# Kernel optimization log

Hardware: AMD Instinct MI355X
Metric: run time of the kernel (lower is better)

Reference implementation:

```python
import jax, jax.numpy as jnp
import numpy as np

B, IN, H, NOPT = 16384, 4096, 128, 64
GAIN = 0.5  # default control_gains value in the module


def gru_cell(x, h, Wih, Whh, bih, bhh):
    # torch GRU single step; gate order r, z, n
    gi = x @ Wih + bih          # [B, 3H]
    gh = h @ Whh + bhh          # [B, 3H]
    ir, iz, inn = jnp.split(gi, 3, axis=-1)
    hr, hz, hn = jnp.split(gh, 3, axis=-1)
    r = jax.nn.sigmoid(ir + hr)
    z = jax.nn.sigmoid(iz + hz)
    n = jnp.tanh(inn + r * hn)
    return (1.0 - z) * n + z * h


def setup_inputs() -> dict:
    key = jax.random.key(0)
    ks = jax.random.split(key, 12)
    s = lambda k, shape: (jax.random.normal(k, shape, jnp.float32) * 0.05)
    return {
        "obs": jax.random.normal(ks[0], (B, IN), jnp.float32),
        "chosen_option": jax.random.randint(ks[1], (B,), 0, NOPT),
        "h0": jnp.zeros((B, H), jnp.float32),
        "h1": jnp.zeros((B, H), jnp.float32),
        "Wa": s(ks[2], (IN, H)), "ba": jnp.zeros((H,), jnp.float32),
        "Wih0": s(ks[3], (H, 3 * H)), "Whh0": s(ks[4], (H, 3 * H)),
        "bih0": jnp.zeros((3 * H,), jnp.float32), "bhh0": jnp.zeros((3 * H,), jnp.float32),
        "Wih1": s(ks[5], (2 * H, 3 * H)), "Whh1": s(ks[6], (H, 3 * H)),
        "bih1": jnp.zeros((3 * H,), jnp.float32), "bhh1": jnp.zeros((3 * H,), jnp.float32),
        "Wv0": s(ks[7], (H, NOPT)), "bv0": jnp.zeros((NOPT,), jnp.float32),
        "Wv1": s(ks[8], (H, NOPT)), "bv1": jnp.zeros((NOPT,), jnp.float32),
        "Wt0": s(ks[9], (H, NOPT)), "bt0": jnp.zeros((NOPT,), jnp.float32),
    }


def reference(obs, chosen_option, h0, h1, Wa, ba, Wih0, Whh0, bih0, bhh0,
              Wih1, Whh1, bih1, bhh1, Wv0, bv0, Wv1, bv1, Wt0, bt0):
    # attention: tanh(Linear(obs))
    attn = jnp.tanh(obs @ Wa + ba)                       # [B, H]
    # layer 0: GRU on attn
    h0n = gru_cell(attn, h0, Wih0, Whh0, bih0, bhh0)     # [B, H]
    hc0 = (h0n - 0.5) * GAIN + 0.5                       # gain contrast
    v0 = hc0 @ Wv0 + bv0                                 # [B, NOPT]
    term = jax.nn.sigmoid(hc0 @ Wt0 + bt0)               # [B, NOPT]
    term_p = jnp.take_along_axis(term, chosen_option[:, None], axis=1)  # [B, 1]
    # layer 1: GRU on cat(attn, own hidden)
    x1 = jnp.concatenate([attn, h1], axis=-1)            # [B, 2H]
    h1n = gru_cell(x1, h1, Wih1, Whh1, bih1, bhh1)       # [B, H]
    hc1 = (h1n - 0.5) * GAIN + 0.5
    v1 = hc1 @ Wv1 + bv1                                 # [B, NOPT]
    return v0, term_p, v1, h0n, h1n
```

## Files before the change

kernel.cpp:

```cpp
#include <hip/hip_runtime.h>
#include <hip/hip_bf16.h>
#include <stdint.h>


typedef __attribute__((ext_vector_type(8))) short bf16x8;
typedef __attribute__((ext_vector_type(4))) float f32x4;
typedef __attribute__((ext_vector_type(8))) float f32x8;

#define INDIM 4096
#define H 128
#define NOPT 64

#define WS_WAT    0u
#define WS_WIH0T  524288u
#define WS_WHH0T  573440u
#define WS_WIH1T  622592u
#define WS_WHH1T  720896u
#define WS_WV0T   770048u
#define WS_WV1T   778240u
#define WS_WT0T   786432u

#define OUT_V0    0u
#define OUT_TERMP 1048576u
#define OUT_V1    1064960u
#define OUT_H0N   2113536u
#define OUT_H1N   4210688u

static __device__ __forceinline__ uint16_t f2bf(float f) {
  __hip_bfloat16 h = __float2bfloat16(f);
  return __builtin_bit_cast(uint16_t, h);
}
static __device__ __forceinline__ float sigm(float x) { return 1.0f / (1.0f + __expf(-x)); }
static __device__ __forceinline__ float fast_tanh(float x) {
  float e = __expf(2.0f * x);
  return 1.0f - 2.0f / (e + 1.0f);
}
static __device__ __forceinline__ f32x4 mfma16(bf16x8 a, bf16x8 b, f32x4 c) {
  return __builtin_amdgcn_mfma_f32_16x16x32_bf16(a, b, c, 0, 0, 0);
}
static __device__ __forceinline__ bf16x8 cvt8(f32x8 v) {
  bf16x8 r;
#pragma unroll
  for (int j = 0; j < 8; ++j) r[j] = (short)f2bf(v[j]);
  return r;
}

__global__ void k_transpose(const float* __restrict__ Wa,
                            const float* __restrict__ Wih0,
                            const float* __restrict__ Whh0,
                            const float* __restrict__ Wih1,
                            const float* __restrict__ Whh1,
                            const float* __restrict__ Wv0,
                            const float* __restrict__ Wv1,
                            const float* __restrict__ Wt0,
                            uint16_t* __restrict__ ws) {
  __shared__ float sT[32][34];
  int blk = blockIdx.x;
  const float* in; uint16_t* out; int K; int N; int base;
  if (blk < 512)      { in = Wa;   out = ws + WS_WAT;   K = 4096; N = 128; base = 0; }
  else if (blk < 560) { in = Wih0; out = ws + WS_WIH0T; K = 128;  N = 384; base = 512; }
  else if (blk < 608) { in = Whh0; out = ws + WS_WHH0T; K = 128;  N = 384; base = 560; }
  else if (blk < 704) { in = Wih1; out = ws + WS_WIH1T; K = 256;  N = 384; base = 608; }
  else if (blk < 752) { in = Whh1; out = ws + WS_WHH1T; K = 128;  N = 384; base = 704; }
  else if (blk < 760) { in = Wv0;  out = ws + WS_WV0T;  K = 128;  N = 64;  base = 752; }
  else if (blk < 768) { in = Wv1;  out = ws + WS_WV1T;  K = 128;  N = 64;  base = 760; }
  else                { in = Wt0;  out = ws + WS_WT0T;  K = 128;  N = 64;  base = 768; }
  const int tix = blk - base;
  const int nTK = K >> 5;
  const int kt = tix & (nTK - 1);
  const int nt = tix / nTK;
  const int k0 = kt * 32, n0 = nt * 32;
  const int t = threadIdx.x;
#pragma unroll
  for (int i = 0; i < 4; ++i) {
    int e = i * 256 + t, kk = e >> 5, nn = e & 31;
    sT[kk][nn] = in[(size_t)(k0 + kk) * N + n0 + nn];
  }
  __syncthreads();
#pragma unroll
  for (int i = 0; i < 4; ++i) {
    int e = i * 256 + t, nn = e >> 5, kk = e & 31;
    out[(size_t)(n0 + nn) * K + k0 + kk] = f2bf(sT[kk][nn]);
  }
}

__launch_bounds__(256, 4)
__global__ void k_fused(const float* __restrict__ obs,
                        const uint16_t* __restrict__ ws,
                        const float* __restrict__ ba,
                        const float* __restrict__ h0,
                        const float* __restrict__ bih0,
                        const float* __restrict__ bhh0,
                        const float* __restrict__ bv0,
                        const float* __restrict__ bt0,
                        const int* __restrict__ chosen,
                        const float* __restrict__ h1,
                        const float* __restrict__ bih1,
                        const float* __restrict__ bhh1,
                        const float* __restrict__ bv1,
                        float* __restrict__ out) {
  __shared__ uint16_t sObs[2][16 * 16 * 8];
  __shared__ uint16_t sX[16 * 16 * 8];
  __shared__ uint16_t sC[16 * 16 * 8];
  const uint16_t* WaT   = ws + WS_WAT;
  const uint16_t* Wih0T = ws + WS_WIH0T;
  const uint16_t* Whh0T = ws + WS_WHH0T;
  const uint16_t* Wih1T = ws + WS_WIH1T;
  const uint16_t* Whh1T = ws + WS_WHH1T;
  const uint16_t* Wv0T  = ws + WS_WV0T;
  const uint16_t* Wv1T  = ws + WS_WV1T;
  const uint16_t* Wt0T  = ws + WS_WT0T;
  const int t = threadIdx.x, w = t >> 6, lane = t & 63;
  const int l15 = lane & 15, quad = lane >> 4;
  const int row0 = blockIdx.x * 16;
  const int nbA = 2 * w;

  f32x4 acc0 = {}, acc1 = {};
  {
    const int r16 = t >> 4;
    const int kb16 = t & 15;
    const float* aptr = obs + (size_t)(row0 + r16) * INDIM + kb16 * 8;
    const int wslot = (r16 * 16 + (kb16 ^ r16)) * 8;
    const uint16_t* brow0 = WaT + (size_t)(nbA * 16 + l15) * INDIM + quad * 8;
    const uint16_t* brow1 = brow0 + (size_t)16 * INDIM;
    f32x8 stg = *(const f32x8*)(aptr);
    for (int kt = 0; kt < 32; ++kt) {
      *(bf16x8*)&sObs[kt & 1][wslot] = cvt8(stg);
      if (kt < 31) stg = *(const f32x8*)(aptr + (size_t)(kt + 1) * 128);
      bf16x8 b[8];
      const int kO = kt * 128;
#pragma unroll
      for (int s = 0; s < 4; ++s) {
        b[s]     = *(const bf16x8*)(brow0 + kO + s * 32);
        b[4 + s] = *(const bf16x8*)(brow1 + kO + s * 32);
      }
      __syncthreads();
#pragma unroll
      for (int s = 0; s < 4; ++s) {
        bf16x8 afr = *(const bf16x8*)&sObs[kt & 1][(l15 * 16 + ((s * 4 + quad) ^ l15)) * 8];
        acc0 = mfma16(afr, b[s], acc0);
        acc1 = mfma16(afr, b[4 + s], acc1);
      }
    }
  }
#pragma unroll
  for (int nbl = 0; nbl < 2; ++nbl) {
    const f32x4 A = nbl ? acc1 : acc0;
    const int col = (nbA + nbl) * 16 + l15;
    const float bav = ba[col];
    const int kb = col >> 3;
#pragma unroll
    for (int i = 0; i < 4; ++i) {
      const int r = quad * 4 + i;
      sX[(r * 16 + (kb ^ r)) * 8 + (col & 7)] = f2bf(fast_tanh(A[i] + bav));
    }
  }
  __syncthreads();

  bf16x8 ax[4], ah[4];
  {
    const float* hrow = h0 + (size_t)(row0 + l15) * H + quad * 8;
#pragma unroll
    for (int ks = 0; ks < 4; ++ks) {
      const int kb = ks * 4 + quad;
      ax[ks] = *(const bf16x8*)&sX[(l15 * 16 + (kb ^ l15)) * 8];
      ah[ks] = cvt8(*(const f32x8*)(hrow + ks * 32));
    }
  }
#pragma unroll
  for (int nbl = 0; nbl < 2; ++nbl) {
    const int nrow = (nbA + nbl) * 16 + l15;
    f32x4 air = {}, ahr = {}, aiz = {}, ahz = {}, ain = {}, ahn = {};
#pragma unroll
    for (int ks = 0; ks < 4; ++ks) {
      const int k = ks * 32 + quad * 8;
      bf16x8 b;
      b = *(const bf16x8*)(Wih0T + (size_t)(nrow      ) * H + k); air = mfma16(ax[ks], b, air);
      b = *(const bf16x8*)(Wih0T + (size_t)(nrow + 128) * H + k); aiz = mfma16(ax[ks], b, aiz);
      b = *(const bf16x8*)(Wih0T + (size_t)(nrow + 256) * H + k); ain = mfma16(ax[ks], b, ain);
      b = *(const bf16x8*)(Whh0T + (size_t)(nrow      ) * H + k); ahr = mfma16(ah[ks], b, ahr);
      b = *(const bf16x8*)(Whh0T + (size_t)(nrow + 128) * H + k); ahz = mfma16(ah[ks], b, ahz);
      b = *(const bf16x8*)(Whh0T + (size_t)(nrow + 256) * H + k); ahn = mfma16(ah[ks], b, ahn);
    }
    const int col = nrow;
    const float b_ir = bih0[col],       b_hr = bhh0[col];
    const float b_iz = bih0[col + 128], b_hz = bhh0[col + 128];
    const float b_in = bih0[col + 256], b_hn = bhh0[col + 256];
    const int kb = col >> 3;
#pragma unroll
    for (int i = 0; i < 4; ++i) {
      const int r = quad * 4 + i;
      const int grow = row0 + r;
      const float rr = sigm(air[i] + ahr[i] + b_ir + b_hr);
      const float zz = sigm(aiz[i] + ahz[i] + b_iz + b_hz);
      const float nn = fast_tanh(ain[i] + b_in + rr * (ahn[i] + b_hn));
      const float hv = h0[(size_t)grow * H + col];
      const float hnew = (1.0f - zz) * nn + zz * hv;
      out[OUT_H0N + (size_t)grow * H + col] = hnew;
      sC[(r * 16 + (kb ^ r)) * 8 + (col & 7)] = f2bf(0.5f * hnew + 0.25f);
    }
  }
  __syncthreads();

  {
    int ch[4];
#pragma unroll
    for (int i = 0; i < 4; ++i) ch[i] = chosen[row0 + quad * 4 + i];
    bf16x8 ac[4];
#pragma unroll
    for (int ks = 0; ks < 4; ++ks) {
      const int kb = ks * 4 + quad;
      ac[ks] = *(const bf16x8*)&sC[(l15 * 16 + (kb ^ l15)) * 8];
    }
    f32x4 av = {}, at = {};
    const int nrow = w * 16 + l15;
#pragma unroll
    for (int ks = 0; ks < 4; ++ks) {
      const int k = ks * 32 + quad * 8;
      bf16x8 b;
      b = *(const bf16x8*)(Wv0T + (size_t)nrow * H + k); av = mfma16(ac[ks], b, av);
      b = *(const bf16x8*)(Wt0T + (size_t)nrow * H + k); at = mfma16(ac[ks], b, at);
    }
    const int col = nrow;
    const float bvv = bv0[col], btv = bt0[col];
#pragma unroll
    for (int i = 0; i < 4; ++i) {
      const int grow = row0 + quad * 4 + i;
      out[OUT_V0 + (size_t)grow * NOPT + col] = av[i] + bvv;
      if (ch[i] == col)
        out[OUT_TERMP + grow] = sigm(at[i] + btv);
    }
  }
  __syncthreads();

  bf16x8 ah1[4];
  {
    const float* hrow = h1 + (size_t)(row0 + l15) * H + quad * 8;
#pragma unroll
    for (int ks = 0; ks < 4; ++ks)
      ah1[ks] = cvt8(*(const f32x8*)(hrow + ks * 32));
  }
#pragma unroll
  for (int nbl = 0; nbl < 2; ++nbl) {
    const int nrow = (nbA + nbl) * 16 + l15;
    f32x4 air = {}, ahr = {}, aiz = {}, ahz = {}, ain = {}, ahn = {};
#pragma unroll
    for (int ks = 0; ks < 8; ++ks) {
      const int k = ks * 32 + quad * 8;
      const bf16x8 a = (ks < 4) ? ax[ks] : ah1[ks - 4];
      bf16x8 b;
      b = *(const bf16x8*)(Wih1T + (size_t)(nrow      ) * 256 + k); air = mfma16(a, b, air);
      b = *(const bf16x8*)(Wih1T + (size_t)(nrow + 128) * 256 + k); aiz = mfma16(a, b, aiz);
      b = *(const bf16x8*)(Wih1T + (size_t)(nrow + 256) * 256 + k); ain = mfma16(a, b, ain);
    }
#pragma unroll
    for (int ks = 0; ks < 4; ++ks) {
      const int k = ks * 32 + quad * 8;
      bf16x8 b;
      b = *(const bf16x8*)(Whh1T + (size_t)(nrow      ) * H + k); ahr = mfma16(ah1[ks], b, ahr);
      b = *(const bf16x8*)(Whh1T + (size_t)(nrow + 128) * H + k); ahz = mfma16(ah1[ks], b, ahz);
      b = *(const bf16x8*)(Whh1T + (size_t)(nrow + 256) * H + k); ahn = mfma16(ah1[ks], b, ahn);
    }
    const int col = nrow;
    const float b_ir = bih1[col],       b_hr = bhh1[col];
    const float b_iz = bih1[col + 128], b_hz = bhh1[col + 128];
    const float b_in = bih1[col + 256], b_hn = bhh1[col + 256];
    const int kb = col >> 3;
#pragma unroll
    for (int i = 0; i < 4; ++i) {
      const int r = quad * 4 + i;
      const int grow = row0 + r;
      const float rr = sigm(air[i] + ahr[i] + b_ir + b_hr);
      const float zz = sigm(aiz[i] + ahz[i] + b_iz + b_hz);
      const float nn = fast_tanh(ain[i] + b_in + rr * (ahn[i] + b_hn));
      const float hv = h1[(size_t)grow * H + col];
      const float hnew = (1.0f - zz) * nn + zz * hv;
      out[OUT_H1N + (size_t)grow * H + col] = hnew;
      sC[(r * 16 + (kb ^ r)) * 8 + (col & 7)] = f2bf(0.5f * hnew + 0.25f);
    }
  }
  __syncthreads();

  {
    bf16x8 ac[4];
#pragma unroll
    for (int ks = 0; ks < 4; ++ks) {
      const int kb = ks * 4 + quad;
      ac[ks] = *(const bf16x8*)&sC[(l15 * 16 + (kb ^ l15)) * 8];
    }
    f32x4 av = {};
    const int nrow = w * 16 + l15;
#pragma unroll
    for (int ks = 0; ks < 4; ++ks) {
      const int k = ks * 32 + quad * 8;
      bf16x8 b = *(const bf16x8*)(Wv1T + (size_t)nrow * H + k);
      av = mfma16(ac[ks], b, av);
    }
    const int col = nrow;
    const float bvv = bv1[col];
#pragma unroll
    for (int i = 0; i < 4; ++i) {
      const int grow = row0 + quad * 4 + i;
      out[OUT_V1 + (size_t)grow * NOPT + col] = av[i] + bvv;
    }
  }
}

extern "C" void kernel_launch(void* const* d_in, const int* in_sizes, int n_in,
                              void* d_out, int out_size, void* d_ws, size_t ws_size,
                              hipStream_t stream) {
  (void)in_sizes; (void)n_in; (void)out_size; (void)ws_size;
  const float* obs    = (const float*)d_in[0];
  const int*   chosen = (const int*)d_in[1];
  const float* h0     = (const float*)d_in[2];
  const float* h1     = (const float*)d_in[3];
  const float* Wa     = (const float*)d_in[4];
  const float* ba     = (const float*)d_in[5];
  const float* Wih0   = (const float*)d_in[6];
  const float* Whh0   = (const float*)d_in[7];
  const float* bih0   = (const float*)d_in[8];
  const float* bhh0   = (const float*)d_in[9];
  const float* Wih1   = (const float*)d_in[10];
  const float* Whh1   = (const float*)d_in[11];
  const float* bih1   = (const float*)d_in[12];
  const float* bhh1   = (const float*)d_in[13];
  const float* Wv0    = (const float*)d_in[14];
  const float* bv0    = (const float*)d_in[15];
  const float* Wv1    = (const float*)d_in[16];
  const float* bv1    = (const float*)d_in[17];
  const float* Wt0    = (const float*)d_in[18];
  const float* bt0    = (const float*)d_in[19];
  uint16_t* ws  = (uint16_t*)d_ws;
  float*    out = (float*)d_out;

  hipLaunchKernelGGL(k_transpose, dim3(776), dim3(256), 0, stream,
                     Wa, Wih0, Whh0, Wih1, Whh1, Wv0, Wv1, Wt0, ws);
  hipLaunchKernelGGL(k_fused, dim3(1024), dim3(256), 0, stream,
                     obs, ws, ba, h0, bih0, bhh0, bv0, bt0, chosen,
                     h1, bih1, bhh1, bv1, out);
}
```

Before: 521.1 us.

## Split fused kernel into attention GEMM and GRU kernels with LDS-staged weights

```diff
diff --git a/kernel.cpp b/kernel.cpp
--- a/kernel.cpp
+++ b/kernel.cpp
@@ -19,12 +19,19 @@
 #define WS_WV0T   770048u
 #define WS_WV1T   778240u
 #define WS_WT0T   786432u
+#define WS_ATTN   794624u
 
 #define OUT_V0    0u
 #define OUT_TERMP 1048576u
 #define OUT_V1    1064960u
 #define OUT_H0N   2113536u
 #define OUT_H1N   4210688u
+
+typedef __attribute__((address_space(1))) const void gas_t;
+typedef __attribute__((address_space(3))) void las_t;
+static __device__ __forceinline__ void gll16(const void* g, void* l) {
+  __builtin_amdgcn_global_load_lds((gas_t*)g, (las_t*)l, 16, 0, 0);
+}
 
 static __device__ __forceinline__ uint16_t f2bf(float f) {
   __hip_bfloat16 h = __float2bfloat16(f);
@@ -85,24 +92,89 @@
 }
 
 __launch_bounds__(256, 4)
-__global__ void k_fused(const float* __restrict__ obs,
-                        const uint16_t* __restrict__ ws,
-                        const float* __restrict__ ba,
-                        const float* __restrict__ h0,
-                        const float* __restrict__ bih0,
-                        const float* __restrict__ bhh0,
-                        const float* __restrict__ bv0,
-                        const float* __restrict__ bt0,
-                        const int* __restrict__ chosen,
-                        const float* __restrict__ h1,
-                        const float* __restrict__ bih1,
-                        const float* __restrict__ bhh1,
-                        const float* __restrict__ bv1,
-                        float* __restrict__ out) {
-  __shared__ uint16_t sObs[2][16 * 16 * 8];
-  __shared__ uint16_t sX[16 * 16 * 8];
-  __shared__ uint16_t sC[16 * 16 * 8];
-  const uint16_t* WaT   = ws + WS_WAT;
+__global__ void k_attn(const float* __restrict__ obs,
+                       uint16_t* __restrict__ ws,
+                       const float* __restrict__ ba) {
+  __shared__ __align__(16) uint16_t sA[2][32 * 8 * 8];
+  __shared__ __align__(16) uint16_t sB[2][128 * 8 * 8];
+  const uint16_t* WaT = ws + WS_WAT;
+  uint16_t* attn = ws + WS_ATTN;
+  const int t = threadIdx.x, w = t >> 6, lane = t & 63;
+  const int l15 = lane & 15, quad = lane >> 4;
+  const int wm = w >> 1, wn = w & 1;
+  const int row0 = blockIdx.x * 32;
+  const int rA = wm * 16 + l15;
+  const int sr = t >> 3, sg = t & 7;
+  const float* aSrc = obs + (size_t)(row0 + sr) * INDIM + sg * 8;
+  const int aDst = (sr * 8 + (sg ^ (sr & 7))) * 8;
+  const int n0 = w * 32 + (lane >> 3);
+  const int gsrc = (lane & 7) ^ (n0 & 7);
+  const uint16_t* bSrc = WaT + (size_t)n0 * INDIM + gsrc * 8;
+
+  f32x4 acc[4] = {};
+
+  auto compute = [&](int buf) {
+#pragma unroll
+    for (int ks = 0; ks < 2; ++ks) {
+      bf16x8 a = *(const bf16x8*)&sA[buf][(rA * 8 + ((ks * 4 + quad) ^ (rA & 7))) * 8];
+#pragma unroll
+      for (int nb = 0; nb < 4; ++nb) {
+        const int n = wn * 64 + nb * 16 + l15;
+        bf16x8 b = *(const bf16x8*)&sB[buf][(n * 8 + ((ks * 4 + quad) ^ (n & 7))) * 8];
+        acc[nb] = mfma16(a, b, acc[nb]);
+      }
+    }
+  };
+
+  {
+    f32x8 av = *(const f32x8*)aSrc;
+#pragma unroll
+    for (int j = 0; j < 4; ++j)
+      gll16(bSrc + (size_t)j * 8 * INDIM, (void*)&sB[0][(w * 4 + j) * 512]);
+    *(bf16x8*)&sA[0][aDst] = cvt8(av);
+  }
+  __syncthreads();
+
+  for (int kt = 0; kt < 63; ++kt) {
+    const int cur = kt & 1, nxt = cur ^ 1;
+    f32x8 av = *(const f32x8*)(aSrc + (size_t)(kt + 1) * 64);
+#pragma unroll
+    for (int j = 0; j < 4; ++j)
+      gll16(bSrc + (size_t)(kt + 1) * 64 + (size_t)j * 8 * INDIM,
+            (void*)&sB[nxt][(w * 4 + j) * 512]);
+    compute(cur);
+    *(bf16x8*)&sA[nxt][aDst] = cvt8(av);
+    __syncthreads();
+  }
+  compute(1);
+
+#pragma unroll
+  for (int nb = 0; nb < 4; ++nb) {
+    const int col = wn * 64 + nb * 16 + l15;
+    const float bav = ba[col];
+#pragma unroll
+    for (int i = 0; i < 4; ++i) {
+      const int r = wm * 16 + quad * 4 + i;
+      attn[(size_t)(row0 + r) * H + col] = f2bf(fast_tanh(acc[nb][i] + bav));
+    }
+  }
+}
+
+__launch_bounds__(512, 4)
+__global__ void k_gru(const uint16_t* __restrict__ ws,
+                      const float* __restrict__ h0,
+                      const float* __restrict__ bih0,
+                      const float* __restrict__ bhh0,
+                      const float* __restrict__ bv0,
+                      const float* __restrict__ bt0,
+                      const int* __restrict__ chosen,
+                      const float* __restrict__ h1,
+                      const float* __restrict__ bih1,
+                      const float* __restrict__ bhh1,
+                      const float* __restrict__ bv1,
+                      float* __restrict__ out) {
+  __shared__ __align__(16) uint16_t sC[64 * 16 * 8];
+  const uint16_t* attn  = ws + WS_ATTN;
   const uint16_t* Wih0T = ws + WS_WIH0T;
   const uint16_t* Whh0T = ws + WS_WHH0T;
   const uint16_t* Wih1T = ws + WS_WIH1T;
@@ -112,64 +184,21 @@
   const uint16_t* Wt0T  = ws + WS_WT0T;
   const int t = threadIdx.x, w = t >> 6, lane = t & 63;
   const int l15 = lane & 15, quad = lane >> 4;
-  const int row0 = blockIdx.x * 16;
-  const int nbA = 2 * w;
-
-  f32x4 acc0 = {}, acc1 = {};
-  {
-    const int r16 = t >> 4;
-    const int kb16 = t & 15;
-    const float* aptr = obs + (size_t)(row0 + r16) * INDIM + kb16 * 8;
-    const int wslot = (r16 * 16 + (kb16 ^ r16)) * 8;
-    const uint16_t* brow0 = WaT + (size_t)(nbA * 16 + l15) * INDIM + quad * 8;
-    const uint16_t* brow1 = brow0 + (size_t)16 * INDIM;
-    f32x8 stg = *(const f32x8*)(aptr);
-    for (int kt = 0; kt < 32; ++kt) {
-      *(bf16x8*)&sObs[kt & 1][wslot] = cvt8(stg);
-      if (kt < 31) stg = *(const f32x8*)(aptr + (size_t)(kt + 1) * 128);
-      bf16x8 b[8];
-      const int kO = kt * 128;
-#pragma unroll
-      for (int s = 0; s < 4; ++s) {
-        b[s]     = *(const bf16x8*)(brow0 + kO + s * 32);
-        b[4 + s] = *(const bf16x8*)(brow1 + kO + s * 32);
-      }
-      __syncthreads();
-#pragma unroll
-      for (int s = 0; s < 4; ++s) {
-        bf16x8 afr = *(const bf16x8*)&sObs[kt & 1][(l15 * 16 + ((s * 4 + quad) ^ l15)) * 8];
-        acc0 = mfma16(afr, b[s], acc0);
-        acc1 = mfma16(afr, b[4 + s], acc1);
-      }
-    }
-  }
-#pragma unroll
-  for (int nbl = 0; nbl < 2; ++nbl) {
-    const f32x4 A = nbl ? acc1 : acc0;
-    const int col = (nbA + nbl) * 16 + l15;
-    const float bav = ba[col];
-    const int kb = col >> 3;
-#pragma unroll
-    for (int i = 0; i < 4; ++i) {
-      const int r = quad * 4 + i;
-      sX[(r * 16 + (kb ^ r)) * 8 + (col & 7)] = f2bf(fast_tanh(A[i] + bav));
-    }
-  }
-  __syncthreads();
+  const int wm = w >> 1, wn = w & 1;
+  const int row0 = blockIdx.x * 64;
+  const int rA = wm * 16 + l15;
 
   bf16x8 ax[4], ah[4];
-  {
-    const float* hrow = h0 + (size_t)(row0 + l15) * H + quad * 8;
-#pragma unroll
-    for (int ks = 0; ks < 4; ++ks) {
-      const int kb = ks * 4 + quad;
-      ax[ks] = *(const bf16x8*)&sX[(l15 * 16 + (kb ^ l15)) * 8];
-      ah[ks] = cvt8(*(const f32x8*)(hrow + ks * 32));
-    }
-  }
-#pragma unroll
-  for (int nbl = 0; nbl < 2; ++nbl) {
-    const int nrow = (nbA + nbl) * 16 + l15;
+#pragma unroll
+  for (int ks = 0; ks < 4; ++ks) {
+    ax[ks] = *(const bf16x8*)(attn + (size_t)(row0 + rA) * H + ks * 32 + quad * 8);
+    ah[ks] = cvt8(*(const f32x8*)(h0 + (size_t)(row0 + rA) * H + ks * 32 + quad * 8));
+  }
+
+#pragma unroll
+  for (int nbl = 0; nbl < 4; ++nbl) {
+    const int nb = wn * 4 + nbl;
+    const int nrow = nb * 16 + l15;
     f32x4 air = {}, ahr = {}, aiz = {}, ahz = {}, ain = {}, ahn = {};
 #pragma unroll
     for (int ks = 0; ks < 4; ++ks) {
@@ -189,7 +218,7 @@
     const int kb = col >> 3;
 #pragma unroll
     for (int i = 0; i < 4; ++i) {
-      const int r = quad * 4 + i;
+      const int r = wm * 16 + quad * 4 + i;
       const int grow = row0 + r;
       const float rr = sigm(air[i] + ahr[i] + b_ir + b_hr);
       const float zz = sigm(aiz[i] + ahz[i] + b_iz + b_hz);
@@ -197,52 +226,52 @@
       const float hv = h0[(size_t)grow * H + col];
       const float hnew = (1.0f - zz) * nn + zz * hv;
       out[OUT_H0N + (size_t)grow * H + col] = hnew;
-      sC[(r * 16 + (kb ^ r)) * 8 + (col & 7)] = f2bf(0.5f * hnew + 0.25f);
+      sC[(r * 16 + (kb ^ (r & 7))) * 8 + (col & 7)] = f2bf(0.5f * hnew + 0.25f);
     }
   }
   __syncthreads();
 
   {
+    bf16x8 ac[4];
+#pragma unroll
+    for (int ks = 0; ks < 4; ++ks)
+      ac[ks] = *(const bf16x8*)&sC[(rA * 16 + ((ks * 4 + quad) ^ (rA & 7))) * 8];
     int ch[4];
 #pragma unroll
-    for (int i = 0; i < 4; ++i) ch[i] = chosen[row0 + quad * 4 + i];
-    bf16x8 ac[4];
-#pragma unroll
-    for (int ks = 0; ks < 4; ++ks) {
-      const int kb = ks * 4 + quad;
-      ac[ks] = *(const bf16x8*)&sC[(l15 * 16 + (kb ^ l15)) * 8];
-    }
-    f32x4 av = {}, at = {};
-    const int nrow = w * 16 + l15;
-#pragma unroll
-    for (int ks = 0; ks < 4; ++ks) {
-      const int k = ks * 32 + quad * 8;
-      bf16x8 b;
-      b = *(const bf16x8*)(Wv0T + (size_t)nrow * H + k); av = mfma16(ac[ks], b, av);
-      b = *(const bf16x8*)(Wt0T + (size_t)nrow * H + k); at = mfma16(ac[ks], b, at);
-    }
-    const int col = nrow;
-    const float bvv = bv0[col], btv = bt0[col];
-#pragma unroll
-    for (int i = 0; i < 4; ++i) {
-      const int grow = row0 + quad * 4 + i;
-      out[OUT_V0 + (size_t)grow * NOPT + col] = av[i] + bvv;
-      if (ch[i] == col)
-        out[OUT_TERMP + grow] = sigm(at[i] + btv);
+    for (int i = 0; i < 4; ++i) ch[i] = chosen[row0 + wm * 16 + quad * 4 + i];
+#pragma unroll
+    for (int hb = 0; hb < 2; ++hb) {
+      const int colf = wn * 2 + hb;
+      const int nrow = colf * 16 + l15;
+      f32x4 av = {}, at = {};
+#pragma unroll
+      for (int ks = 0; ks < 4; ++ks) {
+        const int k = ks * 32 + quad * 8;
+        bf16x8 b;
+        b = *(const bf16x8*)(Wv0T + (size_t)nrow * H + k); av = mfma16(ac[ks], b, av);
+        b = *(const bf16x8*)(Wt0T + (size_t)nrow * H + k); at = mfma16(ac[ks], b, at);
+      }
+      const int col = nrow;
+      const float bvv = bv0[col], btv = bt0[col];
+#pragma unroll
+      for (int i = 0; i < 4; ++i) {
+        const int grow = row0 + wm * 16 + quad * 4 + i;
+        out[OUT_V0 + (size_t)grow * NOPT + col] = av[i] + bvv;
+        if (ch[i] == col)
+          out[OUT_TERMP + grow] = sigm(at[i] + btv);
+      }
     }
   }
   __syncthreads();
 
   bf16x8 ah1[4];
-  {
-    const float* hrow = h1 + (size_t)(row0 + l15) * H + quad * 8;
-#pragma unroll
-    for (int ks = 0; ks < 4; ++ks)
-      ah1[ks] = cvt8(*(const f32x8*)(hrow + ks * 32));
-  }
-#pragma unroll
-  for (int nbl = 0; nbl < 2; ++nbl) {
-    const int nrow = (nbA + nbl) * 16 + l15;
+#pragma unroll
+  for (int ks = 0; ks < 4; ++ks)
+    ah1[ks] = cvt8(*(const f32x8*)(h1 + (size_t)(row0 + rA) * H + ks * 32 + quad * 8));
+#pragma unroll
+  for (int nbl = 0; nbl < 4; ++nbl) {
+    const int nb = wn * 4 + nbl;
+    const int nrow = nb * 16 + l15;
     f32x4 air = {}, ahr = {}, aiz = {}, ahz = {}, ain = {}, ahn = {};
 #pragma unroll
     for (int ks = 0; ks < 8; ++ks) {
@@ -268,7 +297,7 @@
     const int kb = col >> 3;
 #pragma unroll
     for (int i = 0; i < 4; ++i) {
-      const int r = quad * 4 + i;
+      const int r = wm * 16 + quad * 4 + i;
       const int grow = row0 + r;
       const float rr = sigm(air[i] + ahr[i] + b_ir + b_hr);
       const float zz = sigm(aiz[i] + ahz[i] + b_iz + b_hz);
@@ -276,7 +305,7 @@
       const float hv = h1[(size_t)grow * H + col];
       const float hnew = (1.0f - zz) * nn + zz * hv;
       out[OUT_H1N + (size_t)grow * H + col] = hnew;
-      sC[(r * 16 + (kb ^ r)) * 8 + (col & 7)] = f2bf(0.5f * hnew + 0.25f);
+      sC[(r * 16 + (kb ^ (r & 7))) * 8 + (col & 7)] = f2bf(0.5f * hnew + 0.25f);
     }
   }
   __syncthreads();
@@ -284,24 +313,26 @@
   {
     bf16x8 ac[4];
 #pragma unroll
-    for (int ks = 0; ks < 4; ++ks) {
-      const int kb = ks * 4 + quad;
-      ac[ks] = *(const bf16x8*)&sC[(l15 * 16 + (kb ^ l15)) * 8];
-    }
-    f32x4 av = {};
-    const int nrow = w * 16 + l15;
-#pragma unroll
-    for (int ks = 0; ks < 4; ++ks) {
-      const int k = ks * 32 + quad * 8;
-      bf16x8 b = *(const bf16x8*)(Wv1T + (size_t)nrow * H + k);
-      av = mfma16(ac[ks], b, av);
-    }
-    const int col = nrow;
-    const float bvv = bv1[col];
-#pragma unroll
-    for (int i = 0; i < 4; ++i) {
-      const int grow = row0 + quad * 4 + i;
-      out[OUT_V1 + (size_t)grow * NOPT + col] = av[i] + bvv;
+    for (int ks = 0; ks < 4; ++ks)
+      ac[ks] = *(const bf16x8*)&sC[(rA * 16 + ((ks * 4 + quad) ^ (rA & 7))) * 8];
+#pragma unroll
+    for (int hb = 0; hb < 2; ++hb) {
+      const int colf = wn * 2 + hb;
+      const int nrow = colf * 16 + l15;
+      f32x4 av = {};
+#pragma unroll
+      for (int ks = 0; ks < 4; ++ks) {
+        const int k = ks * 32 + quad * 8;
+        bf16x8 b = *(const bf16x8*)(Wv1T + (size_t)nrow * H + k);
+        av = mfma16(ac[ks], b, av);
+      }
+      const int col = nrow;
+      const float bvv = bv1[col];
+#pragma unroll
+      for (int i = 0; i < 4; ++i) {
+        const int grow = row0 + wm * 16 + quad * 4 + i;
+        out[OUT_V1 + (size_t)grow * NOPT + col] = av[i] + bvv;
+      }
     }
   }
 }
@@ -335,7 +366,8 @@
 
   hipLaunchKernelGGL(k_transpose, dim3(776), dim3(256), 0, stream,
                      Wa, Wih0, Whh0, Wih1, Whh1, Wv0, Wv1, Wt0, ws);
-  hipLaunchKernelGGL(k_fused, dim3(1024), dim3(256), 0, stream,
-                     obs, ws, ba, h0, bih0, bhh0, bv0, bt0, chosen,
+  hipLaunchKernelGGL(k_attn, dim3(512), dim3(256), 0, stream, obs, ws, ba);
+  hipLaunchKernelGGL(k_gru, dim3(256), dim3(512), 0, stream,
+                     ws, h0, bih0, bhh0, bv0, bt0, chosen,
                      h1, bih1, bhh1, bv1, out);
 }
```

Result: slower. 540.5 us (+3.7%).
